# Kernel optimization log

Measured on AMD Instinct MI355X. Metric: run time of the kernel, lower is better.

## Reference

```python
import jax, jax.numpy as jnp
import numpy as np

DS = 32          # decoder_size
DIM = 512        # decoder_dim
NH = 8           # num_heads
HD = DIM // NH   # head_size = 64
NE = 4           # num_enc_reshape
NC = 2           # num_classes
B = 8
L = 2            # transformer layers
FF = 4 * DIM


def _ln(x, g, b):
    m = x.mean(-1, keepdims=True)
    v = x.var(-1, keepdims=True)
    return (x - m) / jnp.sqrt(v + 1e-5) * g + b


def _pos_bias(x_emb, y_emb, pad0, pad1):
    # 2D relative position encoding gathered from embeddings, shape [S2,S2,HD]
    ix = jnp.tile(jnp.arange(DS), DS)                       # column index per pixel
    iy = jnp.repeat(jnp.arange(DS), DS)                     # row index per pixel
    xd = jnp.clip(ix[None, :] - ix[:, None], -DS, DS) + DS  # [S2,S2] in [1,2*DS-1]
    yd = jnp.clip(iy[None, :] - iy[:, None], -DS, DS) + DS
    pos = x_emb[xd] + y_emb[yd]                              # [S2,S2,HD]
    S2 = DS * DS
    p0 = jnp.broadcast_to(pad0, (NE, NE, HD))
    p1 = jnp.broadcast_to(pad1, (S2, NE, HD))
    pos_pad = jnp.concatenate([p0, p1], axis=0)              # [S,NE,HD]
    right = jnp.concatenate([jnp.transpose(p1, (1, 0, 2)), pos], axis=0)  # [S,S2,HD]
    return jnp.concatenate([pos_pad, right], axis=1)         # [S,S,HD]


def _forward(x, patches, We, be, x_emb, y_emb, pad0, pad1,
             Wq, bq, Wk, bk, Wv, bv, Wo, bo,
             ln1_g, ln1_b, ln2_g, ln2_b, W1, b1, W2, b2, Wc, bc):
    b = x.shape[0]
    # patch embedding: [B,3,H,W] -> [B,H,W,3] -> Linear(3,DIM) -> [B,S2,DIM]
    p = jnp.transpose(patches, (0, 2, 3, 1))
    px = (p @ We + be).reshape(b, -1, DIM)
    xe = x.reshape(b, NE, DIM)
    h = jnp.concatenate([xe, px], axis=1)                    # [B,S,DIM]
    pos = _pos_bias(x_emb, y_emb, pad0, pad1)                # [S,S,HD]
    scale = 1.0 / jnp.sqrt(jnp.float32(HD))
    for l in range(L):
        hn = _ln(h, ln1_g[l], ln1_b[l])
        q = (hn @ Wq[l] + bq[l]).reshape(b, -1, NH, HD) * scale
        k = (hn @ Wk[l] + bk[l]).reshape(b, -1, NH, HD)
        v = (hn @ Wv[l] + bv[l]).reshape(b, -1, NH, HD)
        # content scores + gathered relative-position structure bias
        scores = jnp.einsum('bihd,bjhd->bhij', q, k) + jnp.einsum('bihd,ijd->bhij', q, pos)
        attn = jax.nn.softmax(scores, axis=-1)
        o = jnp.einsum('bhij,bjhd->bihd', attn, v).reshape(b, -1, DIM)
        h = h + (o @ Wo[l] + bo[l])
        hn = _ln(h, ln2_g[l], ln2_b[l])
        h = h + (jax.nn.relu(hn @ W1[l] + b1[l]) @ W2[l] + b2[l])
    out = h[:, NE:, :] @ Wc + bc                             # [B,S2,NC]
    out = out.reshape(b, DS, DS, NC)
    return jnp.transpose(out, (0, 3, 1, 2))                  # [B,NC,DS,DS]


def setup_inputs() -> dict:
    key = jax.random.key(0)
    ks = jax.random.split(key, 24)
    s = 0.02
    d = {}
    d['x'] = jax.random.normal(ks[0], (B, NE * DIM), jnp.float32)
    d['patches'] = jax.random.normal(ks[1], (B, 3, DS, DS), jnp.float32)
    d['We'] = jax.random.normal(ks[2], (3, DIM), jnp.float32) * s
    d['be'] = jnp.zeros((DIM,), jnp.float32)
    d['x_emb'] = jax.random.normal(ks[3], (2 * DS, HD), jnp.float32) * s
    d['y_emb'] = jax.random.normal(ks[4], (2 * DS, HD), jnp.float32) * s
    d['pad0'] = jax.random.normal(ks[5], (1, 1, HD), jnp.float32) * s
    d['pad1'] = jax.random.normal(ks[6], (1, 1, HD), jnp.float32) * s
    d['Wq'] = jax.random.normal(ks[7], (L, DIM, DIM), jnp.float32) * s
    d['bq'] = jnp.zeros((L, DIM), jnp.float32)
    d['Wk'] = jax.random.normal(ks[8], (L, DIM, DIM), jnp.float32) * s
    d['bk'] = jnp.zeros((L, DIM), jnp.float32)
    d['Wv'] = jax.random.normal(ks[9], (L, DIM, DIM), jnp.float32) * s
    d['bv'] = jnp.zeros((L, DIM), jnp.float32)
    d['Wo'] = jax.random.normal(ks[10], (L, DIM, DIM), jnp.float32) * s
    d['bo'] = jnp.zeros((L, DIM), jnp.float32)
    d['ln1_g'] = jnp.ones((L, DIM), jnp.float32)
    d['ln1_b'] = jnp.zeros((L, DIM), jnp.float32)
    d['ln2_g'] = jnp.ones((L, DIM), jnp.float32)
    d['ln2_b'] = jnp.zeros((L, DIM), jnp.float32)
    d['W1'] = jax.random.normal(ks[11], (L, DIM, FF), jnp.float32) * s
    d['b1'] = jnp.zeros((L, FF), jnp.float32)
    d['W2'] = jax.random.normal(ks[12], (L, FF, DIM), jnp.float32) * s
    d['b2'] = jnp.zeros((L, DIM), jnp.float32)
    d['Wc'] = jax.random.normal(ks[13], (DIM, NC), jnp.float32) * s
    d['bc'] = jnp.zeros((NC,), jnp.float32)
    return d


def reference(x, patches, We, be, x_emb, y_emb, pad0, pad1,
              Wq, bq, Wk, bk, Wv, bv, Wo, bo,
              ln1_g, ln1_b, ln2_g, ln2_b, W1, b1, W2, b2, Wc, bc):
    return _forward(x, patches, We, be, x_emb, y_emb, pad0, pad1,
                    Wq, bq, Wk, bk, Wv, bv, Wo, bo,
                    ln1_g, ln1_b, ln2_g, ln2_b, W1, b1, W2, b2, Wc, bc)
```

## Files before the change

kernel.cpp:

```cpp
#include <hip/hip_runtime.h>
#include <hip/hip_bf16.h>

#define DS 32
#define DIM 512
#define NH 8
#define HD 64
#define NE 4
#define NC 2
#define BB 8
#define LL 2
#define FFD 2048
#define S2 1024
#define SS 1028
#define MM (BB*SS)
#define KE 160
#define EXT ((size_t)BB*NH*SS*KE)
#define WLD 3145728

typedef __attribute__((ext_vector_type(8))) short s16x8;
typedef __attribute__((ext_vector_type(4))) float f32x4;
typedef unsigned short u16;

__device__ __forceinline__ u16 f2b(float f) {
    __hip_bfloat16 h = __float2bfloat16(f);
    return *reinterpret_cast<u16*>(&h);
}
__device__ __forceinline__ float b2f(u16 u) {
    __hip_bfloat16 h;
    *reinterpret_cast<u16*>(&h) = u;
    return __bfloat162float(h);
}

__device__ __forceinline__ void gload_lds16(const void* g, void* l) {
    __builtin_amdgcn_global_load_lds(
        (const __attribute__((address_space(1))) void*)(uintptr_t)g,
        (__attribute__((address_space(3))) void*)(uint32_t)(uintptr_t)l,
        16, 0, 0);
}

__global__ void embed_kernel(const float* __restrict__ x, const float* __restrict__ patches,
                             const float* __restrict__ We, const float* __restrict__ be,
                             float* __restrict__ h) {
    int row = blockIdx.x;
    int b = row / SS, i = row % SS;
    float* hr = h + (size_t)row * DIM;
    if (i < NE) {
        const float* xr = x + (size_t)b*NE*DIM + (size_t)i*DIM;
        for (int d = threadIdx.x; d < DIM; d += blockDim.x) hr[d] = xr[d];
    } else {
        int p = i - NE;
        float c0 = patches[(size_t)b*3*S2 + 0*S2 + p];
        float c1 = patches[(size_t)b*3*S2 + 1*S2 + p];
        float c2 = patches[(size_t)b*3*S2 + 2*S2 + p];
        for (int d = threadIdx.x; d < DIM; d += blockDim.x)
            hr[d] = be[d] + c0*We[d] + c1*We[DIM+d] + c2*We[2*DIM+d];
    }
}

__global__ void ln_kernel(const float* __restrict__ in, u16* __restrict__ out,
                          const float* __restrict__ g, const float* __restrict__ bt) {
    int row = blockIdx.x;
    const float* xr = in + (size_t)row*DIM;
    int t = threadIdx.x;
    float v0 = xr[t], v1 = xr[t+256];
    float s = v0 + v1, s2 = v0*v0 + v1*v1;
    for (int off = 32; off; off >>= 1) { s += __shfl_down(s, off); s2 += __shfl_down(s2, off); }
    __shared__ float ps[4], ps2[4];
    int wid = t >> 6, lane = t & 63;
    if (lane == 0) { ps[wid] = s; ps2[wid] = s2; }
    __syncthreads();
    if (t == 0) { ps[0] = ps[0]+ps[1]+ps[2]+ps[3]; ps2[0] = ps2[0]+ps2[1]+ps2[2]+ps2[3]; }
    __syncthreads();
    float mean = ps[0] * (1.0f/DIM);
    float var  = ps2[0] * (1.0f/DIM) - mean*mean;
    float inv = rsqrtf(var + 1e-5f);
    u16* orow = out + (size_t)row*DIM;
    orow[t]     = f2b((v0 - mean)*inv*g[t]     + bt[t]);
    orow[t+256] = f2b((v1 - mean)*inv*g[t+256] + bt[t+256]);
}

__global__ void transp_all(const float* __restrict__ Wq, const float* __restrict__ Wk,
                           const float* __restrict__ Wv, const float* __restrict__ Wo,
                           const float* __restrict__ W1, const float* __restrict__ W2,
                           u16* __restrict__ wt) {
    int widx = blockIdx.y, l = blockIdx.z;
    const float* src; u16* dst; int R, C;
    u16* base = wt + (size_t)l*WLD;
    if      (widx == 0) { src = Wq + (size_t)l*DIM*DIM; dst = base + 0;       R = DIM; C = DIM; }
    else if (widx == 1) { src = Wk + (size_t)l*DIM*DIM; dst = base + 262144;  R = DIM; C = DIM; }
    else if (widx == 2) { src = Wv + (size_t)l*DIM*DIM; dst = base + 524288;  R = DIM; C = DIM; }
    else if (widx == 3) { src = Wo + (size_t)l*DIM*DIM; dst = base + 786432;  R = DIM; C = DIM; }
    else if (widx == 4) { src = W1 + (size_t)l*DIM*FFD; dst = base + 1048576; R = DIM; C = FFD; }
    else                { src = W2 + (size_t)l*FFD*DIM; dst = base + 2097152; R = FFD; C = DIM; }
    int tilesC = C >> 5;
    int tile = blockIdx.x;
    if (tile >= tilesC * (R >> 5)) return;
    int c0 = (tile % tilesC) * 32, r0 = (tile / tilesC) * 32;
    __shared__ float t_[32][33];
    int tx = threadIdx.x & 31, ty = threadIdx.x >> 5;
    #pragma unroll
    for (int ii = 0; ii < 4; ii++)
        t_[ty + ii*8][tx] = src[(size_t)(r0 + ty + ii*8)*C + c0 + tx];
    __syncthreads();
    #pragma unroll
    for (int ii = 0; ii < 4; ii++)
        dst[(size_t)(c0 + ty + ii*8)*R + r0 + tx] = f2b(t_[tx][ty + ii*8]);
}

__global__ void cat_bias_kernel(const float* __restrict__ bq, const float* __restrict__ bk,
                                const float* __restrict__ bv, float* __restrict__ out) {
    int t = blockIdx.x*256 + threadIdx.x;
    if (t >= 1536) return;
    out[t] = (t < 512) ? bq[t] : (t < 1024 ? bk[t-512] : bv[t-1024]);
}

template<int MODE, int RELU>
__global__ __launch_bounds__(256) void mfma_gemm(
    const u16* __restrict__ A, const u16* __restrict__ WT,
    const float* __restrict__ bias, const float* __restrict__ res,
    float* __restrict__ Cf, u16* __restrict__ Cb,
    u16* __restrict__ kd, u16* __restrict__ vd,
    int M, int N, int K, int Nt)
{
    __shared__ __align__(16) u16 a_lds[2][128*64];
    __shared__ __align__(16) u16 b_lds[2][128*64];
    int nwg = gridDim.x;
    int q8 = nwg >> 3, r8 = nwg & 7;
    int bid = blockIdx.x;
    int xcd = bid & 7, loc = bid >> 3;
    int g = (xcd < r8 ? xcd*(q8+1) : r8*(q8+1) + (xcd - r8)*q8) + loc;
    int row0 = (g / Nt) * 128, col0 = (g % Nt) * 128;

    int tid = threadIdx.x, w = tid>>6, l = tid&63;
    int lg = l>>4, lc = l&15;
    int wr = (w>>1)*64, wc = (w&1)*64;
    f32x4 acc[4][4];
    #pragma unroll
    for (int m = 0; m < 4; m++)
        #pragma unroll
        for (int n = 0; n < 4; n++) { f32x4 z = {0.f,0.f,0.f,0.f}; acc[m][n] = z; }

    int c16 = l & 7;
    auto STAGE = [&](int buf, int kk) {
        #pragma unroll
        for (int p = 0; p < 4; p++) {
            int e = p*256 + tid;
            int r = e >> 3;
            int ra = row0 + r; if (ra > M-1) ra = M-1;
            gload_lds16(A  + (size_t)ra*K + kk + c16*8,          a_lds[buf] + p*2048 + w*512);
            gload_lds16(WT + (size_t)(col0 + r)*K + kk + c16*8,  b_lds[buf] + p*2048 + w*512);
        }
    };

    STAGE(0, 0);
    __syncthreads();
    int nk = K >> 6;
    for (int ki = 0; ki < nk; ki++) {
        int cur = ki & 1;
        if (ki + 1 < nk) STAGE(cur ^ 1, (ki + 1) << 6);
        #pragma unroll
        for (int ks = 0; ks < 2; ks++) {
            int cb = ks*32 + lg*8;
            s16x8 af[4], bfr[4];
            #pragma unroll
            for (int m = 0; m < 4; m++)
                af[m] = *(const s16x8*)(a_lds[cur] + (wr + m*16 + lc)*64 + cb);
            #pragma unroll
            for (int n = 0; n < 4; n++)
                bfr[n] = *(const s16x8*)(b_lds[cur] + (wc + n*16 + lc)*64 + cb);
            #pragma unroll
            for (int m = 0; m < 4; m++)
                #pragma unroll
                for (int n = 0; n < 4; n++)
                    acc[m][n] = __builtin_amdgcn_mfma_f32_16x16x32_bf16(af[m], bfr[n], acc[m][n], 0, 0, 0);
        }
        __syncthreads();
    }
    #pragma unroll
    for (int m = 0; m < 4; m++) {
        #pragma unroll
        for (int r = 0; r < 4; r++) {
            int row = row0 + wr + m*16 + lg*4 + r;
            if (row >= M) continue;
            #pragma unroll
            for (int n = 0; n < 4; n++) {
                int col = col0 + wc + n*16 + lc;
                float v = acc[m][n][r] + bias[col];
                if (MODE == 2) {
                    int which = col >> 9, c2 = col & 511;
                    if (which == 0) v *= 0.125f;
                    u16* dst = (which == 0) ? Cb : (which == 1 ? kd : vd);
                    dst[(size_t)row*512 + c2] = f2b(v);
                } else if (MODE == 1) {
                    if (RELU) v = fmaxf(v, 0.f);
                    Cb[(size_t)row*N + col] = f2b(v);
                } else {
                    Cf[(size_t)row*N + col] = v + res[(size_t)row*N + col];
                }
            }
        }
    }
}

__global__ __launch_bounds__(256) void mfma_gemm_n(
    const u16* __restrict__ A, const u16* __restrict__ WT,
    const float* __restrict__ bias, const float* __restrict__ res,
    float* __restrict__ Cf, int M, int N, int K, int Nt)
{
    __shared__ __align__(16) u16 a_lds[2][64*64];
    __shared__ __align__(16) u16 b_lds[2][128*64];
    int nwg = gridDim.x;
    int q8 = nwg >> 3, r8 = nwg & 7;
    int bid = blockIdx.x;
    int xcd = bid & 7, loc = bid >> 3;
    int g = (xcd < r8 ? xcd*(q8+1) : r8*(q8+1) + (xcd - r8)*q8) + loc;
    int row0 = (g / Nt) * 64, col0 = (g % Nt) * 128;

    int tid = threadIdx.x, w = tid>>6, l = tid&63;
    int lg = l>>4, lc = l&15;
    int wr = (w>>1)*32, wc = (w&1)*64;
    f32x4 acc[2][4];
    #pragma unroll
    for (int m = 0; m < 2; m++)
        #pragma unroll
        for (int n = 0; n < 4; n++) { f32x4 z = {0.f,0.f,0.f,0.f}; acc[m][n] = z; }

    int c16 = l & 7;
    auto STAGE = [&](int buf, int kk) {
        #pragma unroll
        for (int p = 0; p < 2; p++) {
            int e = p*256 + tid;
            int r = e >> 3;
            int ra = row0 + r; if (ra > M-1) ra = M-1;
            gload_lds16(A + (size_t)ra*K + kk + c16*8, a_lds[buf] + p*2048 + w*512);
        }
        #pragma unroll
        for (int p = 0; p < 4; p++) {
            int e = p*256 + tid;
            int r = e >> 3;
            gload_lds16(WT + (size_t)(col0 + r)*K + kk + c16*8, b_lds[buf] + p*2048 + w*512);
        }
    };

    STAGE(0, 0);
    __syncthreads();
    int nk = K >> 6;
    for (int ki = 0; ki < nk; ki++) {
        int cur = ki & 1;
        if (ki + 1 < nk) STAGE(cur ^ 1, (ki + 1) << 6);
        #pragma unroll
        for (int ks = 0; ks < 2; ks++) {
            int cb = ks*32 + lg*8;
            s16x8 af[2], bfr[4];
            #pragma unroll
            for (int m = 0; m < 2; m++)
                af[m] = *(const s16x8*)(a_lds[cur] + (wr + m*16 + lc)*64 + cb);
            #pragma unroll
            for (int n = 0; n < 4; n++)
                bfr[n] = *(const s16x8*)(b_lds[cur] + (wc + n*16 + lc)*64 + cb);
            #pragma unroll
            for (int m = 0; m < 2; m++)
                #pragma unroll
                for (int n = 0; n < 4; n++)
                    acc[m][n] = __builtin_amdgcn_mfma_f32_16x16x32_bf16(af[m], bfr[n], acc[m][n], 0, 0, 0);
        }
        __syncthreads();
    }
    #pragma unroll
    for (int m = 0; m < 2; m++) {
        #pragma unroll
        for (int r = 0; r < 4; r++) {
            int row = row0 + wr + m*16 + lg*4 + r;
            if (row >= M) continue;
            #pragma unroll
            for (int n = 0; n < 4; n++) {
                int col = col0 + wc + n*16 + lc;
                size_t idx = (size_t)row*N + col;
                Cf[idx] = acc[m][n][r] + bias[col] + res[idx];
            }
        }
    }
}

__global__ void qp_kernel(const u16* __restrict__ q, const float* __restrict__ pad0,
                          const float* __restrict__ pad1, float* __restrict__ qp0,
                          float* __restrict__ qp1) {
    int idx = blockIdx.x * blockDim.x + threadIdx.x;
    if (idx >= BB*NH*SS) return;
    int i = idx % SS; int bh = idx / SS; int b = bh >> 3, hh = bh & 7;
    const u16* qr = q + ((size_t)(b*SS + i))*DIM + hh*HD;
    float a0 = 0.f, a1 = 0.f;
    #pragma unroll 8
    for (int d = 0; d < HD; d++) { float qv = b2f(qr[d]); a0 += qv*pad0[d]; a1 += qv*pad1[d]; }
    qp0[idx] = a0; qp1[idx] = a1;
}

__global__ void qext_kernel(const u16* __restrict__ qb, const float* __restrict__ qp0,
                            const float* __restrict__ qp1, u16* __restrict__ Qe) {
    size_t id = (size_t)blockIdx.x*256 + threadIdx.x;
    if (id >= EXT/8) return;
    int u = (int)(id % 20);
    size_t row = id / 20;
    int bh = (int)(row / SS), i = (int)(row - (size_t)bh*SS);
    int b = bh >> 3, hh = bh & 7;
    s16x8 val = {0,0,0,0,0,0,0,0};
    if (u < 8) {
        val = *(const s16x8*)(qb + ((size_t)(b*SS + i))*DIM + hh*HD + u*8);
    } else if (u == 16) {
        float v128 = (i < NE) ? qp0[bh*SS + i] : qp1[bh*SS + i];
        float v129 = (i < NE) ? qp1[bh*SS + i] : 0.f;
        val[0] = (short)f2b(v128);
        val[1] = (short)f2b(v129);
    }
    *(s16x8*)(Qe + row*KE + u*8) = val;
}

__global__ void kext_kernel(const u16* __restrict__ kb, u16* __restrict__ Ke) {
    size_t id = (size_t)blockIdx.x*256 + threadIdx.x;
    if (id >= EXT/8) return;
    int u = (int)(id % 20);
    size_t row = id / 20;
    int bh = (int)(row / SS), j = (int)(row - (size_t)bh*SS);
    int b = bh >> 3, hh = bh & 7;
    const short ONE = 0x3F80;
    s16x8 val = {0,0,0,0,0,0,0,0};
    if (u < 8) {
        val = *(const s16x8*)(kb + ((size_t)(b*SS + j))*DIM + hh*HD + u*8);
    } else {
        int pj = j - NE, cj = pj & 31, rj = pj >> 5;
        #pragma unroll
        for (int e = 0; e < 8; e++) {
            int t = u*8 + e;
            short v = 0;
            if (j >= NE) {
                if (t < 96)       { if (cj == t-64) v = ONE; }
                else if (t < 128) { if (rj == t-96) v = ONE; }
                else if (t == 129) v = ONE;
            } else if (t == 128) v = ONE;
            val[e] = v;
        }
    }
    *(s16x8*)(Ke + row*KE + u*8) = val;
}

__global__ __launch_bounds__(256) void qxy_mfma(
    const u16* __restrict__ q, const float* __restrict__ x_emb,
    const float* __restrict__ y_emb, u16* __restrict__ Qe)
{
    int tile = blockIdx.x, bh = blockIdx.y;
    int b = bh >> 3, hh = bh & 7;
    int tid = threadIdx.x, w = tid>>6, l = tid&63;
    int lg = l>>4, lc = l&15;
    int wr = (w>>1)*64, wc = (w&1)*64;
    int pi0 = tile*128;

    f32x4 acc[4][4];
    #pragma unroll
    for (int m = 0; m < 4; m++)
        #pragma unroll
        for (int n = 0; n < 4; n++) { f32x4 z = {0.f,0.f,0.f,0.f}; acc[m][n] = z; }

    s16x8 af[4][2];
    #pragma unroll
    for (int m = 0; m < 4; m++) {
        int pi = pi0 + wr + m*16 + lc;
        const u16* qp = q + ((size_t)(b*SS + NE + pi))*DIM + hh*HD + lg*8;
        af[m][0] = *(const s16x8*)qp;
        af[m][1] = *(const s16x8*)(qp + 32);
    }
    s16x8 bf[4][2];
    #pragma unroll
    for (int n = 0; n < 4; n++) {
        int tau = wc + n*16 + lc;
        const float* ep = (tau < 64) ? (x_emb + (size_t)tau*HD) : (y_emb + (size_t)(tau-64)*HD);
        #pragma unroll
        for (int ks = 0; ks < 2; ks++) {
            const float* e8 = ep + ks*32 + lg*8;
            s16x8 bv;
            #pragma unroll
            for (int t2 = 0; t2 < 8; t2++) bv[t2] = (short)f2b(e8[t2]);
            bf[n][ks] = bv;
        }
    }
    #pragma unroll
    for (int ks = 0; ks < 2; ks++)
        #pragma unroll
        for (int m = 0; m < 4; m++)
            #pragma unroll
            for (int n = 0; n < 4; n++)
                acc[m][n] = __builtin_amdgcn_mfma_f32_16x16x32_bf16(af[m][ks], bf[n][ks], acc[m][n], 0, 0, 0);

    #pragma unroll
    for (int m = 0; m < 4; m++) {
        #pragma unroll
        for (int r = 0; r < 4; r++) {
            int pi = pi0 + wr + m*16 + lg*4 + r;
            int ci = pi & 31, ri = pi >> 5;
            size_t rowbase = ((size_t)bh*SS + NE + pi)*KE;
            #pragma unroll
            for (int n = 0; n < 4; n++) {
                int tau = wc + n*16 + lc;
                float v = acc[m][n][r];
                if (tau < 64) {
                    int c = tau + ci - 32;
                    if (c >= 0 && c < 32) Qe[rowbase + 64 + c] = f2b(v);
                } else {
                    int c = (tau - 64) + ri - 32;
                    if (c >= 0 && c < 32) Qe[rowbase + 96 + c] = f2b(v);
                }
            }
        }
    }
}

#define KT 64
#define NKT 17
#define NQT 17
__global__ __launch_bounds__(256) void attn_mfma(
    const u16* __restrict__ Qe, const u16* __restrict__ Ke,
    const u16* __restrict__ v, u16* __restrict__ o)
{
    __shared__ __align__(16) u16 Kl[64*192];
    __shared__ __align__(16) u16 Vt[64][72];
    __shared__ __align__(16) u16 Pl[4][16][72];
    int bid = blockIdx.x;
    int g = (bid & 7)*136 + (bid >> 3);
    int qt = g % NQT, bh = g / NQT;
    int b = bh >> 3, hh = bh & 7;
    int tid = threadIdx.x, w = tid>>6, l = tid&63;
    int lg = l>>4, lc = l&15;
    int i0w = qt*64 + w*16;
    const s16x8 zs = {0,0,0,0,0,0,0,0};

    s16x8 qa[5];
    {
        int qrow = i0w + lc; if (qrow > SS-1) qrow = SS-1;
        const u16* qp = Qe + ((size_t)bh*SS + qrow)*KE + lg*8;
        #pragma unroll
        for (int ks = 0; ks < 5; ks++) qa[ks] = *(const s16x8*)(qp + ks*32);
    }

    float m_[4] = {-1e30f, -1e30f, -1e30f, -1e30f};
    float l_[4] = {0.f, 0.f, 0.f, 0.f};
    f32x4 oacc[4];
    #pragma unroll
    for (int f = 0; f < 4; f++) { f32x4 z = {0.f,0.f,0.f,0.f}; oacc[f] = z; }

    int skey = tid & 63, sd0 = (tid >> 6) * 16;

    for (int kt2 = 0; kt2 < NKT; kt2++) {
        int j0 = kt2 * KT;
        #pragma unroll
        for (int p = 0; p < 5; p++) {
            int e = p*256 + tid;
            int row = e / 20, u = e - row*20;
            int j = j0 + row;
            s16x8 kv = zs;
            if (j < SS) kv = *(const s16x8*)(Ke + ((size_t)bh*SS + j)*KE + u*8);
            *(s16x8*)((char*)Kl + row*384 + ((u ^ (row&7)) << 4)) = kv;
        }
        {
            int key = j0 + skey;
            uint4 v0 = {0,0,0,0}, v1 = {0,0,0,0};
            if (key < SS) {
                const uint4* vp = (const uint4*)(v + ((size_t)(b*SS + key))*DIM + hh*HD + sd0);
                v0 = vp[0]; v1 = vp[1];
            }
            const u16* pv = (const u16*)&v0;
            #pragma unroll
            for (int jj = 0; jj < 8; jj++) Vt[sd0 + jj][skey] = pv[jj];
            pv = (const u16*)&v1;
            #pragma unroll
            for (int jj = 0; jj < 8; jj++) Vt[sd0 + 8 + jj][skey] = pv[jj];
        }
        __syncthreads();

        f32x4 s[4];
        #pragma unroll
        for (int f = 0; f < 4; f++) { f32x4 z = {0.f,0.f,0.f,0.f}; s[f] = z; }
        #pragma unroll
        for (int ks = 0; ks < 5; ks++)
            #pragma unroll
            for (int f = 0; f < 4; f++) {
                int row = f*16 + lc;
                s16x8 kb2 = *(const s16x8*)((const char*)Kl + row*384 + ((((ks<<2)+lg) ^ (row&7)) << 4));
                s[f] = __builtin_amdgcn_mfma_f32_16x16x32_bf16(qa[ks], kb2, s[f], 0, 0, 0);
            }

        #pragma unroll
        for (int r = 0; r < 4; r++) {
            #pragma unroll
            for (int f = 0; f < 4; f++) {
                int j = j0 + f*16 + lc;
                if (j >= SS) s[f][r] = -1e30f;
            }
            float t4 = fmaxf(fmaxf(s[0][r], s[1][r]), fmaxf(s[2][r], s[3][r]));
            t4 = fmaxf(t4, __shfl_xor(t4, 1));
            t4 = fmaxf(t4, __shfl_xor(t4, 2));
            t4 = fmaxf(t4, __shfl_xor(t4, 4));
            t4 = fmaxf(t4, __shfl_xor(t4, 8));
            float mn = fmaxf(m_[r], t4);
            float sc = __expf(m_[r] - mn);
            m_[r] = mn;
            float rs = 0.f;
            #pragma unroll
            for (int f = 0; f < 4; f++) {
                float p = __expf(s[f][r] - mn);
                s[f][r] = p;
                rs += p;
            }
            rs += __shfl_xor(rs, 1); rs += __shfl_xor(rs, 2);
            rs += __shfl_xor(rs, 4); rs += __shfl_xor(rs, 8);
            l_[r] = l_[r]*sc + rs;
            #pragma unroll
            for (int f = 0; f < 4; f++) oacc[f][r] *= sc;
        }
        #pragma unroll
        for (int r = 0; r < 4; r++)
            #pragma unroll
            for (int f = 0; f < 4; f++)
                Pl[w][lg*4 + r][f*16 + lc] = f2b(s[f][r]);
        #pragma unroll
        for (int ks = 0; ks < 2; ks++) {
            s16x8 pa = *(const s16x8*)&Pl[w][lc][ks*32 + lg*8];
            #pragma unroll
            for (int f = 0; f < 4; f++) {
                s16x8 vb = *(const s16x8*)&Vt[f*16 + lc][ks*32 + lg*8];
                oacc[f] = __builtin_amdgcn_mfma_f32_16x16x32_bf16(pa, vb, oacc[f], 0, 0, 0);
            }
        }
        __syncthreads();
    }
    #pragma unroll
    for (int r = 0; r < 4; r++) {
        int i = i0w + lg*4 + r;
        if (i >= SS) continue;
        float inv = 1.0f / l_[r];
        #pragma unroll
        for (int f = 0; f < 4; f++)
            o[((size_t)(b*SS + i))*DIM + hh*HD + f*16 + lc] = f2b(oacc[f][r] * inv);
    }
}

__global__ void cls_kernel(const float* __restrict__ h, const float* __restrict__ Wc,
                           const float* __restrict__ bc, float* __restrict__ out) {
    int g = blockIdx.x*4 + (threadIdx.x >> 6);
    int lane = threadIdx.x & 63;
    if (g >= BB*S2) return;
    int b = g >> 10, p = g & 1023;
    const float* hr = h + ((size_t)(b*SS + NE + p))*DIM;
    float a0 = 0.f, a1 = 0.f;
    for (int d = lane; d < DIM; d += 64) {
        float hv = hr[d];
        a0 += hv * Wc[d*NC + 0];
        a1 += hv * Wc[d*NC + 1];
    }
    for (int off = 32; off; off >>= 1) { a0 += __shfl_down(a0, off); a1 += __shfl_down(a1, off); }
    if (lane == 0) {
        out[((size_t)(b*NC + 0))*S2 + p] = a0 + bc[0];
        out[((size_t)(b*NC + 1))*S2 + p] = a1 + bc[1];
    }
}

extern "C" void kernel_launch(void* const* d_in, const int* in_sizes, int n_in,
                              void* d_out, int out_size, void* d_ws, size_t ws_size,
                              hipStream_t stream) {
    const float* x      = (const float*)d_in[0];
    const float* patches= (const float*)d_in[1];
    const float* We     = (const float*)d_in[2];
    const float* be     = (const float*)d_in[3];
    const float* x_emb  = (const float*)d_in[4];
    const float* y_emb  = (const float*)d_in[5];
    const float* pad0   = (const float*)d_in[6];
    const float* pad1   = (const float*)d_in[7];
    const float* Wq     = (const float*)d_in[8];
    const float* bq     = (const float*)d_in[9];
    const float* Wk     = (const float*)d_in[10];
    const float* bk     = (const float*)d_in[11];
    const float* Wv     = (const float*)d_in[12];
    const float* bv     = (const float*)d_in[13];
    const float* Wo     = (const float*)d_in[14];
    const float* bo     = (const float*)d_in[15];
    const float* ln1_g  = (const float*)d_in[16];
    const float* ln1_b  = (const float*)d_in[17];
    const float* ln2_g  = (const float*)d_in[18];
    const float* ln2_b  = (const float*)d_in[19];
    const float* W1     = (const float*)d_in[20];
    const float* b1     = (const float*)d_in[21];
    const float* W2     = (const float*)d_in[22];
    const float* b2     = (const float*)d_in[23];
    const float* Wc     = (const float*)d_in[24];
    const float* bc     = (const float*)d_in[25];
    float* out = (float*)d_out;

    float* ws = (float*)d_ws;
    const size_t MD = (size_t)MM*DIM;
    float* h  = ws;
    u16* hn   = (u16*)(ws + MD);
    u16* qb   = (u16*)(ws + MD + MD/2);
    u16* kb   = qb + MD;
    u16* vb   = qb + 2*MD;
    u16* ob   = qb + 3*MD;
    u16* tb   = qb;
    u16* Qe   = (u16*)(ws + 3*MD + MD/2);
    u16* Ke   = Qe + EXT;
    float* after = ws + 3*MD + MD/2 + EXT;
    float* qp0 = after;
    float* qp1 = qp0 + 65792;
    float* bqkv = qp1 + 65792;
    u16* wt   = (u16*)(bqkv + 1536);

    transp_all<<<dim3(1024, 6, LL), 256, 0, stream>>>(Wq, Wk, Wv, Wo, W1, W2, wt);
    embed_kernel<<<MM, 256, 0, stream>>>(x, patches, We, be, h);

    const int extUnits = (int)(EXT / 8);
    const int extBlocks = (extUnits + 255) / 256;

    for (int l = 0; l < LL; l++) {
        u16* base = wt + (size_t)l*WLD;
        cat_bias_kernel<<<6, 256, 0, stream>>>(bq + (size_t)l*DIM, bk + (size_t)l*DIM, bv + (size_t)l*DIM, bqkv);
        ln_kernel<<<MM, 256, 0, stream>>>(h, hn, ln1_g + l*DIM, ln1_b + l*DIM);
        mfma_gemm<2,0><<<65*12, 256, 0, stream>>>(hn, base, bqkv, nullptr, nullptr, qb, kb, vb, MM, 1536, DIM, 12);
        qp_kernel<<<(BB*NH*SS + 255)/256, 256, 0, stream>>>(qb, pad0, pad1, qp0, qp1);
        qext_kernel<<<extBlocks, 256, 0, stream>>>(qb, qp0, qp1, Qe);
        qxy_mfma<<<dim3(8, BB*NH), 256, 0, stream>>>(qb, x_emb, y_emb, Qe);
        kext_kernel<<<extBlocks, 256, 0, stream>>>(kb, Ke);
        attn_mfma<<<NQT*BB*NH, 256, 0, stream>>>(Qe, Ke, vb, ob);
        mfma_gemm_n<<<129*4, 256, 0, stream>>>(ob, base + 786432, bo + (size_t)l*DIM, h, h, MM, DIM, DIM, 4);
        ln_kernel<<<MM, 256, 0, stream>>>(h, hn, ln2_g + l*DIM, ln2_b + l*DIM);
        mfma_gemm<1,1><<<65*16, 256, 0, stream>>>(hn, base + 1048576, b1 + (size_t)l*FFD, nullptr, nullptr, tb, nullptr, nullptr, MM, FFD, DIM, 16);
        mfma_gemm_n<<<129*4, 256, 0, stream>>>(tb, base + 2097152, b2 + (size_t)l*DIM, h, h, MM, DIM, FFD, 4);
    }

    cls_kernel<<<(BB*S2)/4, 256, 0, stream>>>(h, Wc, bc, out);
}
```

Baseline: 702.2 us.

## Fuse extended Q/K construction into attention kernel, dropping qext/kext passes

Removes the qext and kext kernels that materialized padded 160-wide extended Q and K tensors in global memory. The attention kernel now reads Q and K directly from the projection outputs, reads the compact qxy output (64 wide per row) plus qp0/qp1, and synthesizes the one-hot position columns of K on the fly while filling LDS. This saves two launches per layer and the write and re-read of two large extended buffers. In exchange, the K tile loads do more integer work and issue strided reads from the interleaved q/k layout.

```diff
diff --git a/kernel.cpp b/kernel.cpp
--- a/kernel.cpp
+++ b/kernel.cpp
@@ -14,7 +14,6 @@
 #define SS 1028
 #define MM (BB*SS)
 #define KE 160
-#define EXT ((size_t)BB*NH*SS*KE)
 #define WLD 3145728
 
 typedef __attribute__((ext_vector_type(8))) short s16x8;
@@ -295,57 +294,9 @@
     qp0[idx] = a0; qp1[idx] = a1;
 }
 
-__global__ void qext_kernel(const u16* __restrict__ qb, const float* __restrict__ qp0,
-                            const float* __restrict__ qp1, u16* __restrict__ Qe) {
-    size_t id = (size_t)blockIdx.x*256 + threadIdx.x;
-    if (id >= EXT/8) return;
-    int u = (int)(id % 20);
-    size_t row = id / 20;
-    int bh = (int)(row / SS), i = (int)(row - (size_t)bh*SS);
-    int b = bh >> 3, hh = bh & 7;
-    s16x8 val = {0,0,0,0,0,0,0,0};
-    if (u < 8) {
-        val = *(const s16x8*)(qb + ((size_t)(b*SS + i))*DIM + hh*HD + u*8);
-    } else if (u == 16) {
-        float v128 = (i < NE) ? qp0[bh*SS + i] : qp1[bh*SS + i];
-        float v129 = (i < NE) ? qp1[bh*SS + i] : 0.f;
-        val[0] = (short)f2b(v128);
-        val[1] = (short)f2b(v129);
-    }
-    *(s16x8*)(Qe + row*KE + u*8) = val;
-}
-
-__global__ void kext_kernel(const u16* __restrict__ kb, u16* __restrict__ Ke) {
-    size_t id = (size_t)blockIdx.x*256 + threadIdx.x;
-    if (id >= EXT/8) return;
-    int u = (int)(id % 20);
-    size_t row = id / 20;
-    int bh = (int)(row / SS), j = (int)(row - (size_t)bh*SS);
-    int b = bh >> 3, hh = bh & 7;
-    const short ONE = 0x3F80;
-    s16x8 val = {0,0,0,0,0,0,0,0};
-    if (u < 8) {
-        val = *(const s16x8*)(kb + ((size_t)(b*SS + j))*DIM + hh*HD + u*8);
-    } else {
-        int pj = j - NE, cj = pj & 31, rj = pj >> 5;
-        #pragma unroll
-        for (int e = 0; e < 8; e++) {
-            int t = u*8 + e;
-            short v = 0;
-            if (j >= NE) {
-                if (t < 96)       { if (cj == t-64) v = ONE; }
-                else if (t < 128) { if (rj == t-96) v = ONE; }
-                else if (t == 129) v = ONE;
-            } else if (t == 128) v = ONE;
-            val[e] = v;
-        }
-    }
-    *(s16x8*)(Ke + row*KE + u*8) = val;
-}
-
 __global__ __launch_bounds__(256) void qxy_mfma(
     const u16* __restrict__ q, const float* __restrict__ x_emb,
-    const float* __restrict__ y_emb, u16* __restrict__ Qe)
+    const float* __restrict__ y_emb, u16* __restrict__ qw)
 {
     int tile = blockIdx.x, bh = blockIdx.y;
     int b = bh >> 3, hh = bh & 7;
@@ -396,17 +347,17 @@
         for (int r = 0; r < 4; r++) {
             int pi = pi0 + wr + m*16 + lg*4 + r;
             int ci = pi & 31, ri = pi >> 5;
-            size_t rowbase = ((size_t)bh*SS + NE + pi)*KE;
+            size_t rowbase = ((size_t)bh*S2 + pi)*64;
             #pragma unroll
             for (int n = 0; n < 4; n++) {
                 int tau = wc + n*16 + lc;
                 float v = acc[m][n][r];
                 if (tau < 64) {
                     int c = tau + ci - 32;
-                    if (c >= 0 && c < 32) Qe[rowbase + 64 + c] = f2b(v);
+                    if (c >= 0 && c < 32) qw[rowbase + c] = f2b(v);
                 } else {
                     int c = (tau - 64) + ri - 32;
-                    if (c >= 0 && c < 32) Qe[rowbase + 96 + c] = f2b(v);
+                    if (c >= 0 && c < 32) qw[rowbase + 32 + c] = f2b(v);
                 }
             }
         }
@@ -417,8 +368,10 @@
 #define NKT 17
 #define NQT 17
 __global__ __launch_bounds__(256) void attn_mfma(
-    const u16* __restrict__ Qe, const u16* __restrict__ Ke,
-    const u16* __restrict__ v, u16* __restrict__ o)
+    const u16* __restrict__ qb, const u16* __restrict__ kb,
+    const u16* __restrict__ v, const u16* __restrict__ qw,
+    const float* __restrict__ qp0, const float* __restrict__ qp1,
+    u16* __restrict__ o)
 {
     __shared__ __align__(16) u16 Kl[64*192];
     __shared__ __align__(16) u16 Vt[64][72];
@@ -431,13 +384,25 @@
     int lg = l>>4, lc = l&15;
     int i0w = qt*64 + w*16;
     const s16x8 zs = {0,0,0,0,0,0,0,0};
+    const short ONE = 0x3F80;
 
     s16x8 qa[5];
     {
         int qrow = i0w + lc; if (qrow > SS-1) qrow = SS-1;
-        const u16* qp = Qe + ((size_t)bh*SS + qrow)*KE + lg*8;
-        #pragma unroll
-        for (int ks = 0; ks < 5; ks++) qa[ks] = *(const s16x8*)(qp + ks*32);
+        const u16* qp_ = qb + ((size_t)(b*SS + qrow))*DIM + hh*HD + lg*8;
+        qa[0] = *(const s16x8*)qp_;
+        qa[1] = *(const s16x8*)(qp_ + 32);
+        qa[2] = zs; qa[3] = zs; qa[4] = zs;
+        if (qrow >= NE) {
+            const u16* qwp = qw + ((size_t)bh*S2 + (qrow - NE))*64 + lg*8;
+            qa[2] = *(const s16x8*)qwp;
+            qa[3] = *(const s16x8*)(qwp + 32);
+        }
+        if (lg == 0) {
+            float p0 = qp0[bh*SS + qrow], p1 = qp1[bh*SS + qrow];
+            qa[4][0] = (short)f2b(qrow < NE ? p0 : p1);
+            qa[4][1] = (short)f2b(qrow < NE ? p1 : 0.f);
+        }
     }
 
     float m_[4] = {-1e30f, -1e30f, -1e30f, -1e30f};
@@ -456,7 +421,24 @@
             int row = e / 20, u = e - row*20;
             int j = j0 + row;
             s16x8 kv = zs;
-            if (j < SS) kv = *(const s16x8*)(Ke + ((size_t)bh*SS + j)*KE + u*8);
+            if (j < SS) {
+                if (u < 8) {
+                    kv = *(const s16x8*)(kb + ((size_t)(b*SS + j))*DIM + hh*HD + u*8);
+                } else {
+                    int pj = j - NE, cj = pj & 31, rj = pj >> 5;
+                    #pragma unroll
+                    for (int e8 = 0; e8 < 8; e8++) {
+                        int t = u*8 + e8;
+                        short vv = 0;
+                        if (j >= NE) {
+                            if (t < 96)       { if (cj == t-64) vv = ONE; }
+                            else if (t < 128) { if (rj == t-96) vv = ONE; }
+                            else if (t == 129) vv = ONE;
+                        } else if (t == 128) vv = ONE;
+                        kv[e8] = vv;
+                    }
+                }
+            }
             *(s16x8*)((char*)Kl + row*384 + ((u ^ (row&7)) << 4)) = kv;
         }
         {
@@ -602,19 +584,14 @@
     u16* vb   = qb + 2*MD;
     u16* ob   = qb + 3*MD;
     u16* tb   = qb;
-    u16* Qe   = (u16*)(ws + 3*MD + MD/2);
-    u16* Ke   = Qe + EXT;
-    float* after = ws + 3*MD + MD/2 + EXT;
-    float* qp0 = after;
+    u16* qw   = (u16*)(ws + 3*MD + MD/2);
+    float* qp0 = ws + 3*MD + MD/2 + 2097152;
     float* qp1 = qp0 + 65792;
     float* bqkv = qp1 + 65792;
     u16* wt   = (u16*)(bqkv + 1536);
 
     transp_all<<<dim3(1024, 6, LL), 256, 0, stream>>>(Wq, Wk, Wv, Wo, W1, W2, wt);
     embed_kernel<<<MM, 256, 0, stream>>>(x, patches, We, be, h);
-
-    const int extUnits = (int)(EXT / 8);
-    const int extBlocks = (extUnits + 255) / 256;
 
     for (int l = 0; l < LL; l++) {
         u16* base = wt + (size_t)l*WLD;
@@ -622,10 +599,8 @@
         ln_kernel<<<MM, 256, 0, stream>>>(h, hn, ln1_g + l*DIM, ln1_b + l*DIM);
         mfma_gemm<2,0><<<65*12, 256, 0, stream>>>(hn, base, bqkv, nullptr, nullptr, qb, kb, vb, MM, 1536, DIM, 12);
         qp_kernel<<<(BB*NH*SS + 255)/256, 256, 0, stream>>>(qb, pad0, pad1, qp0, qp1);
-        qext_kernel<<<extBlocks, 256, 0, stream>>>(qb, qp0, qp1, Qe);
-        qxy_mfma<<<dim3(8, BB*NH), 256, 0, stream>>>(qb, x_emb, y_emb, Qe);
-        kext_kernel<<<extBlocks, 256, 0, stream>>>(kb, Ke);
-        attn_mfma<<<NQT*BB*NH, 256, 0, stream>>>(Qe, Ke, vb, ob);
+        qxy_mfma<<<dim3(8, BB*NH), 256, 0, stream>>>(qb, x_emb, y_emb, qw);
+        attn_mfma<<<NQT*BB*NH, 256, 0, stream>>>(qb, kb, vb, qw, qp0, qp1, ob);
         mfma_gemm_n<<<129*4, 256, 0, stream>>>(ob, base + 786432, bo + (size_t)l*DIM, h, h, MM, DIM, DIM, 4);
         ln_kernel<<<MM, 256, 0, stream>>>(h, hn, ln2_g + l*DIM, ln2_b + l*DIM);
         mfma_gemm<1,1><<<65*16, 256, 0, stream>>>(hn, base + 1048576, b1 + (size_t)l*FFD, nullptr, nullptr, tb, nullptr, nullptr, MM, FFD, DIM, 16);
```

Result: slower. 838.3 us (+19.4%).
